# Optimization experiments

Measured on AMD Instinct MI355X. Metric: run time of the kernel, lower is better.

Reference implementation:

```python
import jax, jax.numpy as jnp
import numpy as np

RGB_MEAN = jnp.array([0.4488, 0.4371, 0.404], dtype=jnp.float32)
RGB_RANGE = 255.0
N_FEATS = 64
N_RESBLOCKS = 16
SUPER_OUT = 100 * 16  # full SuperConv2d out_channels
RES_SCALE = 1.0


def conv2d(x, w, b):
    # x: [N,C,H,W], w: [O,I,3,3], SAME padding (pad=1)
    y = jax.lax.conv_general_dilated(
        x, w, window_strides=(1, 1), padding='SAME',
        dimension_numbers=('NCHW', 'OIHW', 'NCHW'))
    return y + b[None, :, None, None]


def setup_inputs() -> dict:
    key = jax.random.key(0)
    ks = jax.random.split(key, 12)
    N, C, H, W = 8, 3, 128, 128
    nf, nrb = N_FEATS, N_RESBLOCKS
    sd = 0.05  # weight std to keep activations bounded over 16 resblocks
    inp = {
        'x': jax.random.normal(ks[0], (N, C, H, W), jnp.float32) * 50.0 + 127.0,
        'head_w': jax.random.normal(ks[1], (nf, C, 3, 3), jnp.float32) * sd,
        'head_b': jnp.zeros((nf,), jnp.float32),
        'rb_w1': jax.random.normal(ks[2], (nrb, nf, nf, 3, 3), jnp.float32) * sd,
        'rb_b1': jnp.zeros((nrb, nf), jnp.float32),
        'rb_w2': jax.random.normal(ks[3], (nrb, nf, nf, 3, 3), jnp.float32) * sd,
        'rb_b2': jnp.zeros((nrb, nf), jnp.float32),
        'body_w': jax.random.normal(ks[4], (nf, nf, 3, 3), jnp.float32) * sd,
        'body_b': jnp.zeros((nf,), jnp.float32),
        'super_w': jax.random.normal(ks[5], (SUPER_OUT, nf, 3, 3), jnp.float32) * sd,
        'super_b': jnp.zeros((SUPER_OUT,), jnp.float32),
        'out_w': jax.random.normal(ks[6], (3, 100, 3, 3), jnp.float32) * sd,
        'out_b': jnp.zeros((3,), jnp.float32),
        'scale': 2,
    }
    return inp


def reference(x, head_w, head_b, rb_w1, rb_b1, rb_w2, rb_b2,
              body_w, body_b, super_w, super_b, out_w, out_b, scale):
    s = int(scale)
    mean = (RGB_RANGE * RGB_MEAN)[None, :, None, None]
    x = x - mean  # sub_mean (std = 1)
    h = conv2d(x, head_w, head_b)  # head: [N,64,H,W]

    def resblock(carry, params):
        w1, b1, w2, b2 = params
        r = jax.nn.relu(conv2d(carry, w1, b1))
        r = conv2d(r, w2, b2)
        return carry + RES_SCALE * r, None

    res, _ = jax.lax.scan(resblock, h, (rb_w1, rb_b1, rb_w2, rb_b2))
    res = conv2d(res, body_w, body_b)
    res = res + h

    # SuperConv2d: dynamic out channels = scale^2 * 100 (slice of full weight)
    out_nc = s * s * 100
    t = conv2d(res, super_w[:out_nc], super_b[:out_nc])  # [N, 100*s^2, H, W]

    # pixel_shuffle: out[i,j,k] = in[i//s, j//s, k*s^2 + (i%s)*s + (j%s)]
    # == standard depth-to-space with channel group ordering (k, a, b)
    N, _, H, W = t.shape
    t = t.reshape(N, 100, s, s, H, W)          # [N,100,a,b,H,W]
    t = t.transpose(0, 1, 4, 2, 5, 3)          # [N,100,H,a,W,b]
    t = t.reshape(N, 100, H * s, W * s)

    y = conv2d(t, out_w, out_b)                # [N,3,H*s,W*s]
    y = y + mean  # add_mean
    return y
```

## Files before the change

kernel.cpp:

```cpp
#include <hip/hip_runtime.h>
#include <hip/hip_bf16.h>

#define HH 128
#define WW 128

typedef _Float16 half2_t __attribute__((ext_vector_type(2)));
typedef _Float16 half4_t __attribute__((ext_vector_type(4)));
typedef _Float16 half8 __attribute__((ext_vector_type(8)));
typedef float f32x4 __attribute__((ext_vector_type(4)));

__global__ __launch_bounds__(256)
void wxform_k(const float* __restrict__ rb_w1, const float* __restrict__ rb_w2,
              const float* __restrict__ body_w, const float* __restrict__ super_w,
              const float* __restrict__ out_w,
              _Float16* __restrict__ Wt, _Float16* __restrict__ Wo) {
    const int per64 = 64 * 64 * 9;
    const int n64   = 33 * per64;
    const int nW    = n64 + 448 * 64 * 9;
    const int total = nW + 1350;
    for (int i = blockIdx.x * 256 + threadIdx.x; i < total; i += gridDim.x * 256) {
        if (i < n64) {
            int l  = i / per64;
            int r  = i - l * per64;
            int ic = r & 63, oc = (r >> 6) & 63, tap = r >> 12;
            const float* src = (l < 16) ? (rb_w1 + (size_t)l * per64)
                             : (l < 32) ? (rb_w2 + (size_t)(l - 16) * per64)
                                        : body_w;
            Wt[i] = (_Float16)src[(oc * 64 + ic) * 9 + tap];
        } else if (i < nW) {
            int r   = i - n64;
            int ic  = r & 63;
            int oc  = (r >> 6) % 448;
            int tap = (r >> 6) / 448;
            float v = (oc < 400) ? super_w[((size_t)oc * 64 + ic) * 9 + tap] : 0.f;
            Wt[i] = (_Float16)v;
        } else {
            int j = i - nW;
            int c = j / 450, r = j - c * 450;
            int p = r / 9, tap = r - p * 9;
            Wo[j * 2]     = (_Float16)out_w[(c * 100 + 2 * p) * 9 + tap];
            Wo[j * 2 + 1] = (_Float16)out_w[(c * 100 + 2 * p + 1) * 9 + tap];
        }
    }
}

__global__ __launch_bounds__(256)
void head_k(const float* __restrict__ x, const float* __restrict__ w,
            const float* __restrict__ b, _Float16* __restrict__ out) {
    int n  = blockIdx.z;
    int gx = blockIdx.x * 16 + (threadIdx.x & 15);
    int gy = blockIdx.y * 16 + (threadIdx.x >> 4);
    float msub[3] = {255.0f * 0.4488f, 255.0f * 0.4371f, 255.0f * 0.4040f};
    float iv[27];
#pragma unroll
    for (int c = 0; c < 3; ++c)
#pragma unroll
        for (int dy = 0; dy < 3; ++dy)
#pragma unroll
            for (int dx = 0; dx < 3; ++dx) {
                int yy = gy + dy - 1, xx = gx + dx - 1;
                float v = 0.f;
                if ((unsigned)yy < HH && (unsigned)xx < WW)
                    v = x[(((size_t)n * 3 + c) * HH + yy) * WW + xx] - msub[c];
                iv[c * 9 + dy * 3 + dx] = v;
            }
    for (int ocg = 0; ocg < 16; ++ocg) {
        half4_t o;
#pragma unroll
        for (int q = 0; q < 4; ++q) {
            int oc  = ocg * 4 + q;
            float a = b[oc];
#pragma unroll
            for (int t = 0; t < 27; ++t) a = fmaf(iv[t], w[oc * 27 + t], a);
            o[q] = (_Float16)a;
        }
        *(half4_t*)&out[((((size_t)n * 16 + ocg) * HH + gy) * WW + gx) * 4] = o;
    }
}

__global__ __launch_bounds__(256, 2)
void frb1_k(const _Float16* __restrict__ in, const _Float16* __restrict__ W1,
            const _Float16* __restrict__ W2, const float* __restrict__ b1,
            const float* __restrict__ b2, _Float16* __restrict__ out) {
    __shared__ __align__(16) _Float16 sBuf[18432 + 18432];
    _Float16* sIn  = sBuf;
    _Float16* sMid = sBuf;
    _Float16* sW   = sBuf + 18432;

    int tid = threadIdx.x;
    int bx = blockIdx.x, by = blockIdx.y, n = blockIdx.z;
    int wv = tid >> 6, lane = tid & 63;
    int lx = lane & 15, lg = lane >> 4;
    int o0 = wv * 4 - 1;
    int g2 = wv & 1;
    int hh = wv >> 1;

    half8 pf[9];
#define PF_W(Wsrc, h)                                                         \
    _Pragma("unroll")                                                         \
    for (int j = 0; j < 9; ++j) {                                             \
        int i = tid + 256 * j;                                                \
        int g = i & 3, oc = (i >> 2) & 63, tap = i >> 8;                      \
        pf[j] = *(const half8*)&Wsrc[(size_t)(tap * 64 + oc) * 64 + (h) * 32 + g * 8]; \
    }
#define WR_W()                                                                \
    _Pragma("unroll")                                                         \
    for (int j = 0; j < 9; ++j) {                                             \
        int i = tid + 256 * j;                                                \
        int g = i & 3, oc = (i >> 2) & 63, tap = i >> 8;                      \
        *(half8*)&sW[(tap * 32 + (oc >> 1)) * 64 +                            \
                     (((g + (oc & 1) * 4) ^ ((oc >> 1) & 7)) << 3)] = pf[j];  \
    }
#define RD_A(tap, oc)                                                         \
    (*(const half8*)&sW[((tap) * 32 + ((oc) >> 1)) * 64 +                     \
                        (((lg + ((oc) & 1) * 4) ^ (((oc) >> 1) & 7)) << 3)])

    PF_W(W1, 0)
    for (int i = tid; i < 2304; i += 256) {
        int icg = i / 288, pl = i - icg * 288;
        int py = pl / 18, px = pl - py * 18;
        int gy = by * 12 + py - 2, gx = bx * 14 + px - 2;
        half8 v = {0, 0, 0, 0, 0, 0, 0, 0};
        if ((unsigned)gy < (unsigned)HH && (unsigned)gx < (unsigned)WW) {
            size_t base = ((((size_t)n * 16 + icg * 2) * HH + gy) * WW + gx) * 4;
            half4_t a = *(const half4_t*)&in[base];
            half4_t c = *(const half4_t*)&in[base + (size_t)HH * WW * 4];
            v[0] = a[0]; v[1] = a[1]; v[2] = a[2]; v[3] = a[3];
            v[4] = c[0]; v[5] = c[1]; v[6] = c[2]; v[7] = c[3];
        }
        *(half8*)&sIn[pl * 64 + ((icg ^ (pl & 7)) << 3)] = v;
    }
    WR_W()
    __syncthreads();

    f32x4 acc1[4][4];
#pragma unroll
    for (int r = 0; r < 4; ++r)
#pragma unroll
        for (int t = 0; t < 4; ++t) acc1[r][t] = (f32x4){0.f, 0.f, 0.f, 0.f};

#define CONV1_CHUNK(h)                                                        \
    {                                                                         \
        _Pragma("unroll")                                                     \
        for (int dx = 0; dx < 3; ++dx) {                                      \
            half8 Bf[6];                                                      \
            _Pragma("unroll")                                                 \
            for (int d = 0; d < 6; ++d) {                                     \
                int pl = (o0 + d + 1) * 18 + (lx + dx);                       \
                Bf[d] = *(const half8*)&sIn[pl * 64 + ((((h) * 4 + lg) ^ (pl & 7)) << 3)]; \
            }                                                                 \
            _Pragma("unroll")                                                 \
            for (int dy = 0; dy < 3; ++dy) {                                  \
                int tap = dy * 3 + dx;                                        \
                half8 Af[4];                                                  \
                _Pragma("unroll")                                             \
                for (int t = 0; t < 4; ++t) Af[t] = RD_A(tap, t * 16 + lx);   \
                _Pragma("unroll")                                             \
                for (int r = 0; r < 4; ++r)                                   \
                    _Pragma("unroll")                                         \
                    for (int t = 0; t < 4; ++t)                               \
                        acc1[r][t] = __builtin_amdgcn_mfma_f32_16x16x32_f16(  \
                            Af[t], Bf[r + dy], acc1[r][t], 0, 0, 0);          \
            }                                                                 \
        }                                                                     \
    }

    PF_W(W1, 1)
    CONV1_CHUNK(0)
    __syncthreads();
    WR_W()
    __syncthreads();
    PF_W(W2, 0)
    CONV1_CHUNK(1)
    half4_t rs[6][2];
#pragma unroll
    for (int r = 0; r < 6; ++r)
#pragma unroll
        for (int t = 0; t < 2; ++t) {
            int oc0 = hh * 32 + t * 16 + lg * 4;
            int pl  = (g2 * 6 + r + 2) * 18 + lx + 2;
            rs[r][t] = *(const half4_t*)&sIn[pl * 64 + (((oc0 >> 3) ^ (pl & 7)) << 3) + (oc0 & 4)];
        }
    __syncthreads();

    {
        int gcol = bx * 14 + lx - 1;
        bool colok = (unsigned)gcol < (unsigned)WW;
#pragma unroll
        for (int r = 0; r < 4; ++r) {
            int o    = o0 + r;
            int grow = by * 12 + o;
            bool ok  = colok && ((unsigned)grow < (unsigned)HH);
#pragma unroll
            for (int t = 0; t < 4; ++t) {
                int oc0 = t * 16 + lg * 4;
                f32x4 bv = *(const f32x4*)&b1[oc0];
                int pl2 = (o + 1) * 18 + lx;
                half4_t ov;
#pragma unroll
                for (int q = 0; q < 4; ++q)
                    ov[q] = ok ? (_Float16)fmaxf(acc1[r][t][q] + bv[q], 0.f)
                               : (_Float16)0.f;
                *(half4_t*)&sMid[pl2 * 64 + (((oc0 >> 3) ^ (pl2 & 7)) << 3) + (oc0 & 4)] = ov;
            }
        }
    }
    WR_W()
    __syncthreads();

    f32x4 acc2[6][2];
#pragma unroll
    for (int r = 0; r < 6; ++r)
#pragma unroll
        for (int t = 0; t < 2; ++t) acc2[r][t] = (f32x4){0.f, 0.f, 0.f, 0.f};

#define CONV2_CHUNK(h)                                                        \
    {                                                                         \
        _Pragma("unroll")                                                     \
        for (int dx = 0; dx < 3; ++dx) {                                      \
            half8 Bf[8];                                                      \
            _Pragma("unroll")                                                 \
            for (int d = 0; d < 8; ++d) {                                     \
                int pl = (g2 * 6 + d) * 18 + (lx + dx);                       \
                Bf[d] = *(const half8*)&sMid[pl * 64 + ((((h) * 4 + lg) ^ (pl & 7)) << 3)]; \
            }                                                                 \
            _Pragma("unroll")                                                 \
            for (int dy = 0; dy < 3; ++dy) {                                  \
                int tap = dy * 3 + dx;                                        \
                half8 Af[2];                                                  \
                _Pragma("unroll")                                             \
                for (int t = 0; t < 2; ++t) Af[t] = RD_A(tap, hh * 32 + t * 16 + lx); \
                _Pragma("unroll")                                             \
                for (int r = 0; r < 6; ++r)                                   \
                    _Pragma("unroll")                                         \
                    for (int t = 0; t < 2; ++t)                               \
                        acc2[r][t] = __builtin_amdgcn_mfma_f32_16x16x32_f16(  \
                            Af[t], Bf[r + dy], acc2[r][t], 0, 0, 0);          \
            }                                                                 \
        }                                                                     \
    }

    PF_W(W2, 1)
    CONV2_CHUNK(0)
    __syncthreads();
    WR_W()
    __syncthreads();
    CONV2_CHUNK(1)
    {
        int gcol = bx * 14 + lx;
        bool sok = (lx < 14) && (gcol < WW);
#pragma unroll
        for (int r = 0; r < 6; ++r) {
            int y = by * 12 + g2 * 6 + r;
            if (!sok || y >= HH) continue;
#pragma unroll
            for (int t = 0; t < 2; ++t) {
                int oc0 = hh * 32 + t * 16 + lg * 4;
                f32x4 bv = *(const f32x4*)&b2[oc0];
                size_t gi = ((((size_t)n * 16 + (oc0 >> 2)) * HH + y) * WW + gcol) * 4;
                half4_t ov;
#pragma unroll
                for (int q = 0; q < 4; ++q)
                    ov[q] = (_Float16)(acc2[r][t][q] + bv[q] + (float)rs[r][t][q]);
                *(half4_t*)&out[gi] = ov;
            }
        }
    }
#undef PF_W
#undef WR_W
#undef RD_A
#undef CONV1_CHUNK
#undef CONV2_CHUNK
}

template<bool RES, bool NT>
__global__ __launch_bounds__(256, 2)
void mconv_k(const _Float16* __restrict__ in, const _Float16* __restrict__ Wt,
             const float* __restrict__ bias, const _Float16* __restrict__ resid,
             _Float16* __restrict__ out, int OCp, int OCr, int C4) {
    __shared__ __align__(16) _Float16 sIn[18 * 18 * 64];
    __shared__ __align__(16) _Float16 sW[9 * 32 * 64];

    int tid = threadIdx.x;
    int n = blockIdx.z, bx = blockIdx.x, by = blockIdx.y;

    for (int i = tid; i < 2592; i += 256) {
        int icg = i / 324, pl = i - icg * 324;
        int py = pl / 18, px = pl - py * 18;
        int gy = by * 16 + py - 1, gx = bx * 16 + px - 1;
        half8 v = {0, 0, 0, 0, 0, 0, 0, 0};
        if ((unsigned)gy < (unsigned)HH && (unsigned)gx < (unsigned)WW) {
            size_t base = ((((size_t)n * 16 + icg * 2) * HH + gy) * WW + gx) * 4;
            half4_t a = *(const half4_t*)&in[base];
            half4_t c = *(const half4_t*)&in[base + (size_t)HH * WW * 4];
            v[0] = a[0]; v[1] = a[1]; v[2] = a[2]; v[3] = a[3];
            v[4] = c[0]; v[5] = c[1]; v[6] = c[2]; v[7] = c[3];
        }
        *(half8*)&sIn[pl * 64 + ((icg ^ (pl & 7)) << 3)] = v;
    }
    __syncthreads();

    int wv = tid >> 6, lane = tid & 63;
    int lx = lane & 15, lg = lane >> 4;
    int r0 = wv * 4;
    int gx0 = bx * 16 + lx;

    for (int ocb = 0; ocb < OCp; ocb += 32) {
        __syncthreads();
        for (int i = tid; i < 2304; i += 256) {
            int tap = i >> 8, oc = (i >> 3) & 31, icg = i & 7;
            half8 v = *(const half8*)&Wt[((size_t)(tap * OCp + ocb + oc)) * 64 + icg * 8];
            *(half8*)&sW[(tap * 32 + oc) * 64 + ((icg ^ (oc & 7)) << 3)] = v;
        }
        __syncthreads();

        f32x4 acc[4][2];
#pragma unroll
        for (int r = 0; r < 4; ++r)
#pragma unroll
            for (int t = 0; t < 2; ++t) acc[r][t] = (f32x4){0.f, 0.f, 0.f, 0.f};

#pragma unroll
        for (int icstep = 0; icstep < 2; ++icstep) {
            int icg = icstep * 4 + lg;
#pragma unroll
            for (int dx = 0; dx < 3; ++dx) {
                half8 Bf[6];
#pragma unroll
                for (int d = 0; d < 6; ++d) {
                    int pl = (r0 + d) * 18 + lx + dx;
                    Bf[d] = *(const half8*)&sIn[pl * 64 + ((icg ^ (pl & 7)) << 3)];
                }
#pragma unroll
                for (int dy = 0; dy < 3; ++dy) {
                    int tap = dy * 3 + dx;
                    half8 Af[2];
#pragma unroll
                    for (int t = 0; t < 2; ++t) {
                        int oc = t * 16 + lx;
                        Af[t] = *(const half8*)&sW[(tap * 32 + oc) * 64 + ((icg ^ (oc & 7)) << 3)];
                    }
#pragma unroll
                    for (int r = 0; r < 4; ++r)
#pragma unroll
                        for (int t = 0; t < 2; ++t)
                            acc[r][t] = __builtin_amdgcn_mfma_f32_16x16x32_f16(
                                Af[t], Bf[r + dy], acc[r][t], 0, 0, 0);
                }
            }
        }
#pragma unroll
        for (int r = 0; r < 4; ++r) {
            int y = by * 16 + r0 + r;
#pragma unroll
            for (int t = 0; t < 2; ++t) {
                int oc0 = ocb + t * 16 + lg * 4;
                if (oc0 >= OCr) continue;
                f32x4 bv = *(const f32x4*)&bias[oc0];
                size_t gi = ((((size_t)n * C4 + (oc0 >> 2)) * HH + y) * WW + gx0) * 4;
                float vv[4];
#pragma unroll
                for (int q = 0; q < 4; ++q) vv[q] = acc[r][t][q] + bv[q];
                if (RES) {
                    half4_t rg = *(const half4_t*)&resid[gi];
#pragma unroll
                    for (int q = 0; q < 4; ++q) vv[q] += (float)rg[q];
                }
                half4_t o;
#pragma unroll
                for (int q = 0; q < 4; ++q) o[q] = (_Float16)vv[q];
                if (NT) __builtin_nontemporal_store(o, (half4_t*)&out[gi]);
                else    *(half4_t*)&out[gi] = o;
            }
        }
    }
}

__global__ __launch_bounds__(256)
void out_k(const _Float16* __restrict__ S, const _Float16* __restrict__ Wo,
           const float* __restrict__ b, float* __restrict__ out) {
    __shared__ __align__(16) _Float16 sG[5 * 324 * 8];
    int n = blockIdx.z;
    int tid = threadIdx.x;
    int ty = tid >> 4, tx = tid & 15;
    int a  = blockIdx.y * 16 + ty;
    int bc = blockIdx.x * 16 + tx;
    float acc[3][2][2];
#pragma unroll
    for (int c = 0; c < 3; ++c)
#pragma unroll
        for (int oy = 0; oy < 2; ++oy)
#pragma unroll
            for (int ox = 0; ox < 2; ++ox) acc[c][oy][ox] = 0.f;

    for (int ch = 0; ch < 10; ++ch) {
        __syncthreads();
        for (int i = tid; i < 1620; i += 256) {
            int p = i / 324, pl = i - p * 324;
            int py = pl / 18, px = pl - py * 18;
            int Y = blockIdx.y * 16 + py - 1, X = blockIdx.x * 16 + px - 1;
            half4_t va = {0, 0, 0, 0}, vc = {0, 0, 0, 0};
            if ((unsigned)Y < 128u && (unsigned)X < 128u) {
                size_t base = ((((size_t)n * 100 + ch * 10 + p * 2) * 128 + Y) * 128 + X) * 4;
                va = *(const half4_t*)&S[base];
                vc = *(const half4_t*)&S[base + (size_t)128 * 128 * 4];
            }
            half8 v;
            v[0] = va[0]; v[1] = vc[0]; v[2] = va[1]; v[3] = vc[1];
            v[4] = va[2]; v[5] = vc[2]; v[6] = va[3]; v[7] = vc[3];
            *(half8*)&sG[(p * 324 + pl) * 8] = v;
        }
        __syncthreads();
#pragma unroll
        for (int p = 0; p < 5; ++p) {
            half2_t wv[3][9];
#pragma unroll
            for (int c = 0; c < 3; ++c)
#pragma unroll
                for (int t = 0; t < 9; ++t)
                    wv[c][t] = *(const half2_t*)&Wo[((c * 50 + ch * 5 + p) * 9 + t) * 2];
            half8 G[3][3];
#pragma unroll
            for (int yi = 0; yi < 3; ++yi)
#pragma unroll
                for (int xi = 0; xi < 3; ++xi)
                    G[yi][xi] = *(const half8*)&sG[(p * 324 + (ty + yi) * 18 + tx + xi) * 8];
#pragma unroll
            for (int oy = 0; oy < 2; ++oy)
#pragma unroll
                for (int ox = 0; ox < 2; ++ox)
#pragma unroll
                    for (int dy = 0; dy < 3; ++dy)
#pragma unroll
                        for (int dx = 0; dx < 3; ++dx) {
                            const int ey = oy + dy - 1, ex = ox + dx - 1;
                            const int yi = (ey >> 1) + 1, xi = (ex >> 1) + 1;
                            const int sub = (ey & 1) * 2 + (ex & 1);
                            half8 g8 = G[yi][xi];
                            half2_t gp = {g8[2 * sub], g8[2 * sub + 1]};
#pragma unroll
                            for (int c = 0; c < 3; ++c)
                                acc[c][oy][ox] = __builtin_amdgcn_fdot2(
                                    gp, wv[c][dy * 3 + dx], acc[c][oy][ox], false);
                        }
        }
    }
    const float madd[3] = {255.0f * 0.4488f, 255.0f * 0.4371f, 255.0f * 0.4040f};
#pragma unroll
    for (int c = 0; c < 3; ++c)
#pragma unroll
        for (int oy = 0; oy < 2; ++oy)
#pragma unroll
            for (int ox = 0; ox < 2; ++ox)
                out[(((size_t)n * 3 + c) * 256 + 2 * a + oy) * 256 + 2 * bc + ox] =
                    acc[c][oy][ox] + b[c] + madd[c];
}

extern "C" void kernel_launch(void* const* d_in, const int* in_sizes, int n_in,
                              void* d_out, int out_size, void* d_ws, size_t ws_size,
                              hipStream_t stream) {
    const float* x       = (const float*)d_in[0];
    const float* head_w  = (const float*)d_in[1];
    const float* head_b  = (const float*)d_in[2];
    const float* rb_w1   = (const float*)d_in[3];
    const float* rb_b1   = (const float*)d_in[4];
    const float* rb_w2   = (const float*)d_in[5];
    const float* rb_b2   = (const float*)d_in[6];
    const float* body_w  = (const float*)d_in[7];
    const float* body_b  = (const float*)d_in[8];
    const float* super_w = (const float*)d_in[9];
    const float* super_b = (const float*)d_in[10];
    const float* out_w   = (const float*)d_in[11];
    const float* out_b   = (const float*)d_in[12];
    float* out = (float*)d_out;

    const size_t ACT = (size_t)16777216;
    char* wsb = (char*)d_ws;
    _Float16* Tb = (_Float16*)wsb;
    _Float16* Hb = (_Float16*)(wsb + ACT);
    _Float16* Cb = (_Float16*)(wsb + 2 * ACT);
    _Float16* Sb = (_Float16*)(wsb + ACT);
    _Float16* Wt = (_Float16*)(wsb + ACT + 104857600);
    _Float16* Wo = (_Float16*)(wsb + ACT + 104857600 + 2949120);

    wxform_k<<<dim3(1440), 256, 0, stream>>>(rb_w1, rb_w2, body_w, super_w,
                                             out_w, Wt, Wo);

    head_k<<<dim3(8, 8, 8), 256, 0, stream>>>(x, head_w, head_b, Hb);

    const _Float16* Wt_bod = Wt + (size_t)32 * 36864;
    const _Float16* Wt_sup = Wt + (size_t)33 * 36864;

    const _Float16* cur = Hb;
    for (int i = 0; i < 16; ++i) {
        _Float16* dst = (i & 1) ? Cb : Tb;
        frb1_k<<<dim3(10, 11, 8), 256, 0, stream>>>(
            cur, Wt + (size_t)i * 36864, Wt + (size_t)(16 + i) * 36864,
            rb_b1 + i * 64, rb_b2 + i * 64, dst);
        cur = dst;
    }
    mconv_k<true, false><<<dim3(8, 8, 8), 256, 0, stream>>>(
        Cb, Wt_bod, body_b, Hb, Tb, 64, 64, 16);
    mconv_k<false, true><<<dim3(8, 8, 8), 256, 0, stream>>>(
        Tb, Wt_sup, super_b, nullptr, Sb, 448, 400, 100);
    out_k<<<dim3(8, 8, 8), 256, 0, stream>>>(Sb, Wo, out_b, out);
}
```

Baseline: 918.1 us.

## Split resblock weight staging into quarter chunks and widen mconv blocks

The fused resblock kernel now stages weights in 32-input by 32-output-channel quarters instead of 64-output halves. It narrows the spatial tile from 14 to 13 columns, which cuts shared memory enough to target three blocks per CU instead of two. Each wave's conv2 work is changed to 3 rows across all 64 output channels. The mconv kernel moves to 512-thread blocks with 2 rows per wave to expose more waves. In exchange, the resblock kernel pays for more barriers, more weight reloads and a smaller share of useful columns per tile.

```diff
diff --git a/kernel.cpp b/kernel.cpp
--- a/kernel.cpp
+++ b/kernel.cpp
@@ -78,48 +78,51 @@
     }
 }
 
-__global__ __launch_bounds__(256, 2)
+__global__ __launch_bounds__(256, 3)
 void frb1_k(const _Float16* __restrict__ in, const _Float16* __restrict__ W1,
             const _Float16* __restrict__ W2, const float* __restrict__ b1,
             const float* __restrict__ b2, _Float16* __restrict__ out) {
-    __shared__ __align__(16) _Float16 sBuf[18432 + 18432];
+    __shared__ __align__(16) _Float16 sBuf[17408 + 9216];
     _Float16* sIn  = sBuf;
     _Float16* sMid = sBuf;
-    _Float16* sW   = sBuf + 18432;
+    _Float16* sW   = sBuf + 17408;
 
     int tid = threadIdx.x;
     int bx = blockIdx.x, by = blockIdx.y, n = blockIdx.z;
     int wv = tid >> 6, lane = tid & 63;
     int lx = lane & 15, lg = lane >> 4;
     int o0 = wv * 4 - 1;
-    int g2 = wv & 1;
-    int hh = wv >> 1;
-
-    half8 pf[9];
-#define PF_W(Wsrc, h)                                                         \
+    int m0 = wv * 3;
+
+    half8 pf[5];
+#define PF_W(Wsrc, icoff, ocoff)                                              \
     _Pragma("unroll")                                                         \
-    for (int j = 0; j < 9; ++j) {                                             \
+    for (int j = 0; j < 5; ++j) {                                             \
         int i = tid + 256 * j;                                                \
-        int g = i & 3, oc = (i >> 2) & 63, tap = i >> 8;                      \
-        pf[j] = *(const half8*)&Wsrc[(size_t)(tap * 64 + oc) * 64 + (h) * 32 + g * 8]; \
+        if (i < 1152) {                                                       \
+            int g = i & 3, ocl = (i >> 2) & 31, tap = i >> 7;                 \
+            pf[j] = *(const half8*)&Wsrc[(size_t)(tap * 64 + (ocoff) + ocl) * 64 + (icoff) + g * 8]; \
+        }                                                                     \
     }
 #define WR_W()                                                                \
     _Pragma("unroll")                                                         \
-    for (int j = 0; j < 9; ++j) {                                             \
+    for (int j = 0; j < 5; ++j) {                                             \
         int i = tid + 256 * j;                                                \
-        int g = i & 3, oc = (i >> 2) & 63, tap = i >> 8;                      \
-        *(half8*)&sW[(tap * 32 + (oc >> 1)) * 64 +                            \
-                     (((g + (oc & 1) * 4) ^ ((oc >> 1) & 7)) << 3)] = pf[j];  \
+        if (i < 1152) {                                                       \
+            int g = i & 3, ocl = (i >> 2) & 31, tap = i >> 7;                 \
+            *(half8*)&sW[(tap * 16 + (ocl >> 1)) * 64 +                       \
+                         (((g + (ocl & 1) * 4) ^ ((ocl >> 1) & 7)) << 3)] = pf[j]; \
+        }                                                                     \
     }
 #define RD_A(tap, oc)                                                         \
-    (*(const half8*)&sW[((tap) * 32 + ((oc) >> 1)) * 64 +                     \
+    (*(const half8*)&sW[((tap) * 16 + ((oc) >> 1)) * 64 +                     \
                         (((lg + ((oc) & 1) * 4) ^ (((oc) >> 1) & 7)) << 3)])
 
-    PF_W(W1, 0)
-    for (int i = tid; i < 2304; i += 256) {
-        int icg = i / 288, pl = i - icg * 288;
-        int py = pl / 18, px = pl - py * 18;
-        int gy = by * 12 + py - 2, gx = bx * 14 + px - 2;
+    PF_W(W1, 0, 0)
+    for (int i = tid; i < 2176; i += 256) {
+        int icg = i / 272, pl = i - icg * 272;
+        int py = pl / 17, px = pl - py * 17;
+        int gy = by * 12 + py - 2, gx = bx * 13 + px - 2;
         half8 v = {0, 0, 0, 0, 0, 0, 0, 0};
         if ((unsigned)gy < (unsigned)HH && (unsigned)gx < (unsigned)WW) {
             size_t base = ((((size_t)n * 16 + icg * 2) * HH + gy) * WW + gx) * 4;
@@ -139,129 +142,130 @@
 #pragma unroll
         for (int t = 0; t < 4; ++t) acc1[r][t] = (f32x4){0.f, 0.f, 0.f, 0.f};
 
-#define CONV1_CHUNK(h)                                                        \
+#define CONV1_CHUNK(ch, os)                                                   \
     {                                                                         \
         _Pragma("unroll")                                                     \
         for (int dx = 0; dx < 3; ++dx) {                                      \
             half8 Bf[6];                                                      \
             _Pragma("unroll")                                                 \
             for (int d = 0; d < 6; ++d) {                                     \
-                int pl = (o0 + d + 1) * 18 + (lx + dx);                       \
-                Bf[d] = *(const half8*)&sIn[pl * 64 + ((((h) * 4 + lg) ^ (pl & 7)) << 3)]; \
-            }                                                                 \
-            _Pragma("unroll")                                                 \
-            for (int dy = 0; dy < 3; ++dy) {                                  \
-                int tap = dy * 3 + dx;                                        \
-                half8 Af[4];                                                  \
-                _Pragma("unroll")                                             \
-                for (int t = 0; t < 4; ++t) Af[t] = RD_A(tap, t * 16 + lx);   \
-                _Pragma("unroll")                                             \
-                for (int r = 0; r < 4; ++r)                                   \
-                    _Pragma("unroll")                                         \
-                    for (int t = 0; t < 4; ++t)                               \
-                        acc1[r][t] = __builtin_amdgcn_mfma_f32_16x16x32_f16(  \
-                            Af[t], Bf[r + dy], acc1[r][t], 0, 0, 0);          \
-            }                                                                 \
-        }                                                                     \
-    }
-
-    PF_W(W1, 1)
-    CONV1_CHUNK(0)
-    __syncthreads();
-    WR_W()
-    __syncthreads();
-    PF_W(W2, 0)
-    CONV1_CHUNK(1)
-    half4_t rs[6][2];
-#pragma unroll
-    for (int r = 0; r < 6; ++r)
-#pragma unroll
-        for (int t = 0; t < 2; ++t) {
-            int oc0 = hh * 32 + t * 16 + lg * 4;
-            int pl  = (g2 * 6 + r + 2) * 18 + lx + 2;
-            rs[r][t] = *(const half4_t*)&sIn[pl * 64 + (((oc0 >> 3) ^ (pl & 7)) << 3) + (oc0 & 4)];
-        }
-    __syncthreads();
-
-    {
-        int gcol = bx * 14 + lx - 1;
-        bool colok = (unsigned)gcol < (unsigned)WW;
-#pragma unroll
-        for (int r = 0; r < 4; ++r) {
-            int o    = o0 + r;
-            int grow = by * 12 + o;
-            bool ok  = colok && ((unsigned)grow < (unsigned)HH);
-#pragma unroll
-            for (int t = 0; t < 4; ++t) {
-                int oc0 = t * 16 + lg * 4;
-                f32x4 bv = *(const f32x4*)&b1[oc0];
-                int pl2 = (o + 1) * 18 + lx;
-                half4_t ov;
-#pragma unroll
-                for (int q = 0; q < 4; ++q)
-                    ov[q] = ok ? (_Float16)fmaxf(acc1[r][t][q] + bv[q], 0.f)
-                               : (_Float16)0.f;
-                *(half4_t*)&sMid[pl2 * 64 + (((oc0 >> 3) ^ (pl2 & 7)) << 3) + (oc0 & 4)] = ov;
-            }
-        }
-    }
-    WR_W()
-    __syncthreads();
-
-    f32x4 acc2[6][2];
-#pragma unroll
-    for (int r = 0; r < 6; ++r)
-#pragma unroll
-        for (int t = 0; t < 2; ++t) acc2[r][t] = (f32x4){0.f, 0.f, 0.f, 0.f};
-
-#define CONV2_CHUNK(h)                                                        \
-    {                                                                         \
-        _Pragma("unroll")                                                     \
-        for (int dx = 0; dx < 3; ++dx) {                                      \
-            half8 Bf[8];                                                      \
-            _Pragma("unroll")                                                 \
-            for (int d = 0; d < 8; ++d) {                                     \
-                int pl = (g2 * 6 + d) * 18 + (lx + dx);                       \
-                Bf[d] = *(const half8*)&sMid[pl * 64 + ((((h) * 4 + lg) ^ (pl & 7)) << 3)]; \
+                int pl = (o0 + d + 1) * 17 + (lx + dx);                       \
+                Bf[d] = *(const half8*)&sIn[pl * 64 + ((((ch) + lg) ^ (pl & 7)) << 3)]; \
             }                                                                 \
             _Pragma("unroll")                                                 \
             for (int dy = 0; dy < 3; ++dy) {                                  \
                 int tap = dy * 3 + dx;                                        \
                 half8 Af[2];                                                  \
                 _Pragma("unroll")                                             \
-                for (int t = 0; t < 2; ++t) Af[t] = RD_A(tap, hh * 32 + t * 16 + lx); \
+                for (int t = 0; t < 2; ++t) Af[t] = RD_A(tap, t * 16 + lx);   \
                 _Pragma("unroll")                                             \
-                for (int r = 0; r < 6; ++r)                                   \
+                for (int r = 0; r < 4; ++r)                                   \
                     _Pragma("unroll")                                         \
                     for (int t = 0; t < 2; ++t)                               \
-                        acc2[r][t] = __builtin_amdgcn_mfma_f32_16x16x32_f16(  \
-                            Af[t], Bf[r + dy], acc2[r][t], 0, 0, 0);          \
+                        acc1[r][(os) + t] = __builtin_amdgcn_mfma_f32_16x16x32_f16( \
+                            Af[t], Bf[r + dy], acc1[r][(os) + t], 0, 0, 0);   \
             }                                                                 \
         }                                                                     \
     }
 
-    PF_W(W2, 1)
-    CONV2_CHUNK(0)
+    PF_W(W1, 0, 32)  CONV1_CHUNK(0, 0) __syncthreads();
+    WR_W()           __syncthreads();
+    PF_W(W1, 32, 0)  CONV1_CHUNK(0, 2) __syncthreads();
+    WR_W()           __syncthreads();
+    PF_W(W1, 32, 32) CONV1_CHUNK(4, 0) __syncthreads();
+    WR_W()           __syncthreads();
+    PF_W(W2, 0, 0)   CONV1_CHUNK(4, 2)
+    half4_t rs[3][4];
+#pragma unroll
+    for (int rr = 0; rr < 3; ++rr)
+#pragma unroll
+        for (int c = 0; c < 4; ++c) {
+            int oc0 = c * 16 + lg * 4;
+            int pl  = (m0 + rr + 2) * 17 + lx + 2;
+            rs[rr][c] = *(const half4_t*)&sIn[pl * 64 + (((oc0 >> 3) ^ (pl & 7)) << 3) + (oc0 & 4)];
+        }
     __syncthreads();
+
+    {
+        int gcol = bx * 13 + lx - 1;
+        bool colok = (unsigned)gcol < (unsigned)WW;
+#pragma unroll
+        for (int r = 0; r < 4; ++r) {
+            int o    = o0 + r;
+            int grow = by * 12 + o;
+            bool ok  = colok && ((unsigned)grow < (unsigned)HH);
+#pragma unroll
+            for (int c = 0; c < 4; ++c) {
+                int oc0 = c * 16 + lg * 4;
+                f32x4 bv = *(const f32x4*)&b1[oc0];
+                int pl2 = (o + 1) * 17 + lx;
+                half4_t ov;
+#pragma unroll
+                for (int q = 0; q < 4; ++q)
+                    ov[q] = ok ? (_Float16)fmaxf(acc1[r][c][q] + bv[q], 0.f)
+                               : (_Float16)0.f;
+                *(half4_t*)&sMid[pl2 * 64 + (((oc0 >> 3) ^ (pl2 & 7)) << 3) + (oc0 & 4)] = ov;
+            }
+        }
+    }
     WR_W()
     __syncthreads();
-    CONV2_CHUNK(1)
+
+    f32x4 acc2[3][4];
+#pragma unroll
+    for (int rr = 0; rr < 3; ++rr)
+#pragma unroll
+        for (int t = 0; t < 4; ++t) acc2[rr][t] = (f32x4){0.f, 0.f, 0.f, 0.f};
+
+#define CONV2_CHUNK(ch, os)                                                   \
+    {                                                                         \
+        _Pragma("unroll")                                                     \
+        for (int dx = 0; dx < 3; ++dx) {                                      \
+            half8 Bf[5];                                                      \
+            _Pragma("unroll")                                                 \
+            for (int d = 0; d < 5; ++d) {                                     \
+                int pl = (m0 + d) * 17 + (lx + dx);                           \
+                Bf[d] = *(const half8*)&sMid[pl * 64 + ((((ch) + lg) ^ (pl & 7)) << 3)]; \
+            }                                                                 \
+            _Pragma("unroll")                                                 \
+            for (int dy = 0; dy < 3; ++dy) {                                  \
+                int tap = dy * 3 + dx;                                        \
+                half8 Af[2];                                                  \
+                _Pragma("unroll")                                             \
+                for (int t = 0; t < 2; ++t) Af[t] = RD_A(tap, t * 16 + lx);   \
+                _Pragma("unroll")                                             \
+                for (int rr = 0; rr < 3; ++rr)                                \
+                    _Pragma("unroll")                                         \
+                    for (int t = 0; t < 2; ++t)                               \
+                        acc2[rr][(os) + t] = __builtin_amdgcn_mfma_f32_16x16x32_f16( \
+                            Af[t], Bf[rr + dy], acc2[rr][(os) + t], 0, 0, 0); \
+            }                                                                 \
+        }                                                                     \
+    }
+
+    PF_W(W2, 0, 32)  CONV2_CHUNK(0, 0) __syncthreads();
+    WR_W()           __syncthreads();
+    PF_W(W2, 32, 0)  CONV2_CHUNK(0, 2) __syncthreads();
+    WR_W()           __syncthreads();
+    PF_W(W2, 32, 32) CONV2_CHUNK(4, 0) __syncthreads();
+    WR_W()           __syncthreads();
+    CONV2_CHUNK(4, 2)
     {
-        int gcol = bx * 14 + lx;
-        bool sok = (lx < 14) && (gcol < WW);
-#pragma unroll
-        for (int r = 0; r < 6; ++r) {
-            int y = by * 12 + g2 * 6 + r;
+        int gcol = bx * 13 + lx;
+        bool sok = (lx < 13) && (gcol < WW);
+#pragma unroll
+        for (int rr = 0; rr < 3; ++rr) {
+            int y = by * 12 + m0 + rr;
             if (!sok || y >= HH) continue;
 #pragma unroll
-            for (int t = 0; t < 2; ++t) {
-                int oc0 = hh * 32 + t * 16 + lg * 4;
+            for (int c = 0; c < 4; ++c) {
+                int oc0 = c * 16 + lg * 4;
                 f32x4 bv = *(const f32x4*)&b2[oc0];
                 size_t gi = ((((size_t)n * 16 + (oc0 >> 2)) * HH + y) * WW + gcol) * 4;
                 half4_t ov;
 #pragma unroll
                 for (int q = 0; q < 4; ++q)
-                    ov[q] = (_Float16)(acc2[r][t][q] + bv[q] + (float)rs[r][t][q]);
+                    ov[q] = (_Float16)(acc2[rr][c][q] + bv[q] + (float)rs[rr][c][q]);
                 *(half4_t*)&out[gi] = ov;
             }
         }
@@ -274,7 +278,7 @@
 }
 
 template<bool RES, bool NT>
-__global__ __launch_bounds__(256, 2)
+__global__ __launch_bounds__(512, 2)
 void mconv_k(const _Float16* __restrict__ in, const _Float16* __restrict__ Wt,
              const float* __restrict__ bias, const _Float16* __restrict__ resid,
              _Float16* __restrict__ out, int OCp, int OCr, int C4) {
@@ -284,7 +288,7 @@
     int tid = threadIdx.x;
     int n = blockIdx.z, bx = blockIdx.x, by = blockIdx.y;
 
-    for (int i = tid; i < 2592; i += 256) {
+    for (int i = tid; i < 2592; i += 512) {
         int icg = i / 324, pl = i - icg * 324;
         int py = pl / 18, px = pl - py * 18;
         int gy = by * 16 + py - 1, gx = bx * 16 + px - 1;
@@ -302,21 +306,21 @@
 
     int wv = tid >> 6, lane = tid & 63;
     int lx = lane & 15, lg = lane >> 4;
-    int r0 = wv * 4;
+    int r0 = wv * 2;
     int gx0 = bx * 16 + lx;
 
     for (int ocb = 0; ocb < OCp; ocb += 32) {
         __syncthreads();
-        for (int i = tid; i < 2304; i += 256) {
+        for (int i = tid; i < 2304; i += 512) {
             int tap = i >> 8, oc = (i >> 3) & 31, icg = i & 7;
             half8 v = *(const half8*)&Wt[((size_t)(tap * OCp + ocb + oc)) * 64 + icg * 8];
             *(half8*)&sW[(tap * 32 + oc) * 64 + ((icg ^ (oc & 7)) << 3)] = v;
         }
         __syncthreads();
 
-        f32x4 acc[4][2];
-#pragma unroll
-        for (int r = 0; r < 4; ++r)
+        f32x4 acc[2][2];
+#pragma unroll
+        for (int r = 0; r < 2; ++r)
 #pragma unroll
             for (int t = 0; t < 2; ++t) acc[r][t] = (f32x4){0.f, 0.f, 0.f, 0.f};
 
@@ -325,9 +329,9 @@
             int icg = icstep * 4 + lg;
 #pragma unroll
             for (int dx = 0; dx < 3; ++dx) {
-                half8 Bf[6];
-#pragma unroll
-                for (int d = 0; d < 6; ++d) {
+                half8 Bf[4];
+#pragma unroll
+                for (int d = 0; d < 4; ++d) {
                     int pl = (r0 + d) * 18 + lx + dx;
                     Bf[d] = *(const half8*)&sIn[pl * 64 + ((icg ^ (pl & 7)) << 3)];
                 }
@@ -341,7 +345,7 @@
                         Af[t] = *(const half8*)&sW[(tap * 32 + oc) * 64 + ((icg ^ (oc & 7)) << 3)];
                     }
 #pragma unroll
-                    for (int r = 0; r < 4; ++r)
+                    for (int r = 0; r < 2; ++r)
 #pragma unroll
                         for (int t = 0; t < 2; ++t)
                             acc[r][t] = __builtin_amdgcn_mfma_f32_16x16x32_f16(
@@ -350,7 +354,7 @@
             }
         }
 #pragma unroll
-        for (int r = 0; r < 4; ++r) {
+        for (int r = 0; r < 2; ++r) {
             int y = by * 16 + r0 + r;
 #pragma unroll
             for (int t = 0; t < 2; ++t) {
@@ -499,9 +503,9 @@
             rb_b1 + i * 64, rb_b2 + i * 64, dst);
         cur = dst;
     }
-    mconv_k<true, false><<<dim3(8, 8, 8), 256, 0, stream>>>(
+    mconv_k<true, false><<<dim3(8, 8, 8), 512, 0, stream>>>(
         Cb, Wt_bod, body_b, Hb, Tb, 64, 64, 16);
-    mconv_k<false, true><<<dim3(8, 8, 8), 256, 0, stream>>>(
+    mconv_k<false, true><<<dim3(8, 8, 8), 512, 0, stream>>>(
         Tb, Wt_sup, super_b, nullptr, Sb, 448, 400, 100);
     out_k<<<dim3(8, 8, 8), 256, 0, stream>>>(Sb, Wo, out_b, out);
 }
```

Measured after the change: 1.294 ms. +41.0%, slower.
